# Performance work log

Hardware: AMD Instinct MI355X
Metric: run time of the kernel (lower is better)

The kernel has to match this reference:

```python
import jax, jax.numpy as jnp
import numpy as np

HID = 1024
HEADS = 16
HEAD_DIM = HID // HEADS
INTER = 4 * HID
EPS = 1e-6
SCALE = 1.0 / np.sqrt(HEAD_DIM)


def setup_inputs() -> dict:
    key = jax.random.key(0)
    ks = jax.random.split(key, 8)
    s = 0.02
    return {
        "x": jax.random.normal(ks[0], (2, 2048, HID), dtype=jnp.float32),
        "wq": jax.random.normal(ks[1], (HID, HID), dtype=jnp.float32) * s,
        "wk": jax.random.normal(ks[2], (HID, HID), dtype=jnp.float32) * s,
        "wv": jax.random.normal(ks[3], (HID, HID), dtype=jnp.float32) * s,
        "wo": jax.random.normal(ks[4], (HID, HID), dtype=jnp.float32) * s,
        "w_gate": jax.random.normal(ks[5], (INTER, HID), dtype=jnp.float32) * s,
        "w_up": jax.random.normal(ks[6], (INTER, HID), dtype=jnp.float32) * s,
        "w_down": jax.random.normal(ks[7], (HID, INTER), dtype=jnp.float32) * s,
        "norm1_w": jnp.ones((HID,), dtype=jnp.float32),
        "norm2_w": jnp.ones((HID,), dtype=jnp.float32),
    }


def _rmsnorm(x, w):
    rms = jnp.sqrt(jnp.mean(x * x, axis=-1, keepdims=True) + EPS)
    return x / rms * w


def reference(x, wq, wk, wv, wo, w_gate, w_up, w_down, norm1_w, norm2_w):
    b, s, _ = x.shape
    residual = x
    h = _rmsnorm(x, norm1_w)
    # projections: nn.Linear computes h @ W.T
    q = (h @ wq.T).reshape(b, s, HEADS, HEAD_DIM).transpose(0, 2, 1, 3)
    k = (h @ wk.T).reshape(b, s, HEADS, HEAD_DIM).transpose(0, 2, 1, 3)
    v = (h @ wv.T).reshape(b, s, HEADS, HEAD_DIM).transpose(0, 2, 1, 3)
    scores = jnp.einsum("bhqd,bhkd->bhqk", q, k) * SCALE
    attn = jax.nn.softmax(scores, axis=-1)
    out = jnp.einsum("bhqk,bhkd->bhqd", attn, v)
    out = out.transpose(0, 2, 1, 3).reshape(b, s, HID)
    x = residual + out @ wo.T
    residual = x
    h = _rmsnorm(x, norm2_w)
    gate = jax.nn.silu(h @ w_gate.T)
    up = h @ w_up.T
    mlp_out = (gate * up) @ w_down.T
    return residual + mlp_out
```

## Files before the change

kernel.cpp:

```cpp
#include <hip/hip_runtime.h>
#include <hip/hip_bf16.h>

#define HID 1024
#define SEQ 2048
#define NTOK 4096
#define ATT_SCALE 0.125f

typedef __attribute__((ext_vector_type(4))) float f32x4;
typedef __attribute__((ext_vector_type(16))) float f32x16;
typedef __attribute__((ext_vector_type(8))) __bf16 bf16x8;
typedef __attribute__((ext_vector_type(4))) __bf16 bf16x4;
typedef __bf16 bf16;

__device__ __forceinline__ bf16 f2bf(float f) { return (bf16)f; }

__device__ __forceinline__ void gld_lds16(const void* g, void* l) {
  __builtin_amdgcn_global_load_lds((const __attribute__((address_space(1))) void*)g,
                                   (__attribute__((address_space(3))) void*)l,
                                   16, 0, 0);
}

__device__ __forceinline__ f32x4 mfma16(bf16x8 a, bf16x8 b, f32x4 c) {
  return __builtin_amdgcn_mfma_f32_16x16x32_bf16(a, b, c, 0, 0, 0);
}
__device__ __forceinline__ f32x16 mfma32(bf16x8 a, bf16x8 b, f32x16 c) {
  return __builtin_amdgcn_mfma_f32_32x32x16_bf16(a, b, c, 0, 0, 0);
}

struct CvtArgs {
  const float* src[7];
  bf16* dst[7];
};

__global__ __launch_bounds__(256) void cvt_weights(CvtArgs a) {
  const int g = blockIdx.x * 256 + threadIdx.x;
  const int s = g >> 18;
  const int seg = s < 4 ? s : (s < 8 ? 4 : (s < 12 ? 5 : 6));
  const int start = seg < 4 ? (seg << 18) : (((seg - 4) << 20) + (1 << 20));
  const int loc = (g - start) << 2;
  const float4 v = *(const float4*)(a.src[seg] + loc);
  bf16x4 o = {f2bf(v.x), f2bf(v.y), f2bf(v.z), f2bf(v.w)};
  *(bf16x4*)(a.dst[seg] + loc) = o;
}

__global__ __launch_bounds__(256) void rmsnorm_k(const float* __restrict__ x,
                                                 const float* __restrict__ w,
                                                 bf16* __restrict__ h) {
  const int row = blockIdx.x;
  const int tid = threadIdx.x;
  const float4 xv = *(const float4*)(x + (size_t)row * HID + tid * 4);
  float ss = xv.x * xv.x + xv.y * xv.y + xv.z * xv.z + xv.w * xv.w;
#pragma unroll
  for (int m = 1; m < 64; m <<= 1) ss += __shfl_xor(ss, m, 64);
  __shared__ float wsum[4];
  if ((tid & 63) == 0) wsum[tid >> 6] = ss;
  __syncthreads();
  const float tot = wsum[0] + wsum[1] + wsum[2] + wsum[3];
  const float inv = rsqrtf(tot * (1.0f / HID) + 1e-6f);
  const float4 wv = *(const float4*)(w + tid * 4);
  bf16x4 o = {f2bf(xv.x * inv * wv.x), f2bf(xv.y * inv * wv.y),
              f2bf(xv.z * inv * wv.z), f2bf(xv.w * inv * wv.w)};
  *(bf16x4*)(h + (size_t)row * HID + tid * 4) = o;
}

template <int EPI>
__global__ __launch_bounds__(256) void gemm_bt(const bf16* __restrict__ A, int lda,
                                               const bf16* __restrict__ B, int ldb,
                                               void* __restrict__ C,
                                               const float* __restrict__ R,
                                               int ldc, int K) {
  alignas(16) __shared__ bf16 As[128 * 32];
  alignas(16) __shared__ bf16 Bs[128 * 32];
  const int tid = threadIdx.x;
  const int wid = tid >> 6;
  const int lane = tid & 63;
  const int bm0 = blockIdx.y * 128;
  const int bn0 = blockIdx.x * 128;
  const int wr = wid >> 1, wc = wid & 1;

  f32x4 acc[4][4] = {};

  const int sr = tid >> 2;
  const int sc = (tid & 3) << 3;
  const bf16* gA = A + (size_t)(bm0 + sr) * lda + sc;
  const bf16* gB = B + (size_t)(bn0 + sr) * ldb + sc;
  bf16* lA = As + wid * 512;
  bf16* lB = Bs + wid * 512;
  const int frow = lane & 15;
  const int kofs = (lane >> 4) << 3;

  for (int k0 = 0; k0 < K; k0 += 32) {
    __syncthreads();
    gld_lds16(gA + k0, lA);
    gld_lds16(gA + k0 + (size_t)64 * lda, lA + 2048);
    gld_lds16(gB + k0, lB);
    gld_lds16(gB + k0 + (size_t)64 * ldb, lB + 2048);
    __syncthreads();
    bf16x8 af[4], bfr[4];
#pragma unroll
    for (int m = 0; m < 4; ++m)
      af[m] = *(const bf16x8*)(As + (wr * 64 + m * 16 + frow) * 32 + kofs);
#pragma unroll
    for (int n = 0; n < 4; ++n)
      bfr[n] = *(const bf16x8*)(Bs + (wc * 64 + n * 16 + frow) * 32 + kofs);
#pragma unroll
    for (int m = 0; m < 4; ++m)
#pragma unroll
      for (int n = 0; n < 4; ++n)
        acc[m][n] = mfma16(af[m], bfr[n], acc[m][n]);
  }

  const int er = bm0 + wr * 64 + ((lane >> 4) << 2);
  const int ec = bn0 + wc * 64 + (lane & 15);
#pragma unroll
  for (int m = 0; m < 4; ++m)
#pragma unroll
    for (int n = 0; n < 4; ++n)
#pragma unroll
      for (int r = 0; r < 4; ++r) {
        const size_t idx = (size_t)(er + m * 16 + r) * ldc + (ec + n * 16);
        if (EPI == 0) ((bf16*)C)[idx] = f2bf(acc[m][n][r]);
        else          ((float*)C)[idx] = R[idx] + acc[m][n][r];
      }
}

__global__ __launch_bounds__(256) void vtrans_k(const bf16* __restrict__ qkv,
                                                bf16* __restrict__ vt) {
  const int bh = blockIdx.y;
  const int b = bh >> 4, head = bh & 15;
  const int st0 = blockIdx.x * 64;
  const int wid = threadIdx.x >> 6, lane = threadIdx.x & 63;
  const bf16* src = qkv + ((size_t)b * SEQ + st0 + lane) * 3072 + 2 * HID + head * 64 + wid * 16;
  bf16* dst = vt + (size_t)bh * (64 * SEQ) + st0 + lane;
#pragma unroll
  for (int half = 0; half < 2; ++half) {
    bf16x8 v = *(const bf16x8*)(src + half * 8);
#pragma unroll
    for (int i = 0; i < 8; ++i)
      dst[(size_t)(wid * 16 + half * 8 + i) * SEQ] = v[i];
  }
}

__global__ __launch_bounds__(128) void attn_k(const bf16* __restrict__ qkv,
                                              const bf16* __restrict__ vt,
                                              bf16* __restrict__ attn_out) {
  const int bh = blockIdx.y;
  const int b = bh >> 4, head = bh & 15;
  const int tid = threadIdx.x, wid = tid >> 6, lane = tid & 63;
  const int l31 = lane & 31, h = lane >> 5;
  const int r7 = l31 & 7;

  alignas(16) __shared__ bf16 Ks[64 * 64];
  alignas(16) __shared__ bf16 Vs[64 * 64];

  const size_t tokq = (size_t)b * SEQ + blockIdx.x * 64 + wid * 32 + l31;
  bf16x8 qf[4];
#pragma unroll
  for (int s = 0; s < 4; ++s) {
    bf16x8 t = *(const bf16x8*)(qkv + tokq * 3072 + head * 64 + s * 16 + h * 8);
#pragma unroll
    for (int i = 0; i < 8; ++i) t[i] = f2bf((float)t[i] * ATT_SCALE);
    qf[s] = t;
  }

  const int sr = tid >> 1;
  const int sc = (tid & 1) * 32;
  const int p5 = sr & 31;
  const int keyr = (sr & 32) | (p5 & 16) | (((p5 >> 2) & 1) << 3) | (((p5 >> 3) & 1) << 2) | (p5 & 3);
  const bf16* kg = qkv + ((size_t)b * SEQ + keyr) * 3072 + HID + head * 64 + sc;
  const bf16* vg = vt + (size_t)bh * (64 * SEQ) + (size_t)sr * SEQ + sc;
  int wofs[4];
#pragma unroll
  for (int j = 0; j < 4; ++j)
    wofs[j] = sr * 64 + ((((sc >> 3) + j) ^ (sr & 7)) << 3);

  f32x16 o0 = {}, o1 = {};
  float m = -1e30f, l = 0.f;

  for (int t0 = 0; t0 < SEQ; t0 += 64) {
    __syncthreads();
#pragma unroll
    for (int j = 0; j < 4; ++j) {
      bf16x8 kv = *(const bf16x8*)(kg + (size_t)t0 * 3072 + j * 8);
      *(bf16x8*)(Ks + wofs[j]) = kv;
      bf16x8 vv = *(const bf16x8*)(vg + t0 + j * 8);
      *(bf16x8*)(Vs + wofs[j]) = vv;
    }
    __syncthreads();

    f32x16 s0 = {}, s1 = {};
#pragma unroll
    for (int s = 0; s < 4; ++s) {
      bf16x8 k0 = *(const bf16x8*)(Ks + l31 * 64 + (((2 * s + h) ^ r7) << 3));
      s0 = mfma32(k0, qf[s], s0);
      bf16x8 k1 = *(const bf16x8*)(Ks + (32 + l31) * 64 + (((2 * s + h) ^ r7) << 3));
      s1 = mfma32(k1, qf[s], s1);
    }

    float pmax = s0[0];
#pragma unroll
    for (int i = 1; i < 16; ++i) pmax = fmaxf(pmax, s0[i]);
#pragma unroll
    for (int i = 0; i < 16; ++i) pmax = fmaxf(pmax, s1[i]);
    pmax = fmaxf(pmax, __shfl_xor(pmax, 32, 64));
    const float mnew = fmaxf(m, pmax);
    const float al = __expf(m - mnew);
    m = mnew;

    bf16x8 pa[4];
    float sum = 0.f;
#pragma unroll
    for (int t = 0; t < 2; ++t)
#pragma unroll
      for (int j = 0; j < 8; ++j) {
        const float p = __expf(s0[8 * t + j] - mnew);
        sum += p;
        pa[t][j] = f2bf(p);
      }
#pragma unroll
    for (int t = 0; t < 2; ++t)
#pragma unroll
      for (int j = 0; j < 8; ++j) {
        const float p = __expf(s1[8 * t + j] - mnew);
        sum += p;
        pa[2 + t][j] = f2bf(p);
      }
    sum += __shfl_xor(sum, 32, 64);
    l = l * al + sum;
#pragma unroll
    for (int i = 0; i < 16; ++i) { o0[i] *= al; o1[i] *= al; }

#pragma unroll
    for (int t = 0; t < 4; ++t) {
      bf16x8 v0 = *(const bf16x8*)(Vs + l31 * 64 + (((2 * t + h) ^ r7) << 3));
      o0 = mfma32(v0, pa[t], o0);
      bf16x8 v1 = *(const bf16x8*)(Vs + (32 + l31) * 64 + (((2 * t + h) ^ r7) << 3));
      o1 = mfma32(v1, pa[t], o1);
    }
  }

  const float inv = 1.0f / l;
  bf16* obase = attn_out + tokq * HID + head * 64;
#pragma unroll
  for (int rq = 0; rq < 4; ++rq) {
    bf16x4 w0, w1;
#pragma unroll
    for (int i = 0; i < 4; ++i) {
      w0[i] = f2bf(o0[4 * rq + i] * inv);
      w1[i] = f2bf(o1[4 * rq + i] * inv);
    }
    *(bf16x4*)(obase + 8 * rq + 4 * h) = w0;
    *(bf16x4*)(obase + 32 + 8 * rq + 4 * h) = w1;
  }
}

__global__ __launch_bounds__(256) void silu_mul_k(bf16* __restrict__ gu) {
  const int t = blockIdx.x * 256 + threadIdx.x;
  const int row = t >> 9;
  const int j = (t & 511) << 3;
  bf16* p = gu + (size_t)row * 8192 + j;
  bf16x8 g8 = *(const bf16x8*)p;
  bf16x8 u8 = *(const bf16x8*)(p + 4096);
  bf16x8 o;
#pragma unroll
  for (int i = 0; i < 8; ++i) {
    const float g = (float)g8[i], u = (float)u8[i];
    const float s = g / (1.0f + __expf(-g));
    o[i] = f2bf(s * u);
  }
  *(bf16x8*)p = o;
}

extern "C" void kernel_launch(void* const* d_in, const int* in_sizes, int n_in,
                              void* d_out, int out_size, void* d_ws, size_t ws_size,
                              hipStream_t stream) {
  const float* x  = (const float*)d_in[0];
  const float* wq = (const float*)d_in[1];
  const float* wk = (const float*)d_in[2];
  const float* wv = (const float*)d_in[3];
  const float* wo = (const float*)d_in[4];
  const float* wg = (const float*)d_in[5];
  const float* wu = (const float*)d_in[6];
  const float* wd = (const float*)d_in[7];
  const float* n1 = (const float*)d_in[8];
  const float* n2 = (const float*)d_in[9];

  char* ws = (char*)d_ws;
  bf16* wqkv_b  = (bf16*)(ws);
  bf16* wo_b    = (bf16*)(ws + 6291456);
  bf16* wgu_b   = (bf16*)(ws + 8388608);
  bf16* wd_b    = (bf16*)(ws + 25165824);
  bf16* h       = (bf16*)(ws + 33554432);
  bf16* attnout = (bf16*)(ws + 41943040);
  bf16* qkv     = (bf16*)(ws + 50331648);
  bf16* vt      = (bf16*)(ws + 75497472);
  bf16* gu      = (bf16*)(ws + 50331648);
  float* x2     = (float*)d_out;

  CvtArgs ca;
  ca.src[0] = wq; ca.dst[0] = wqkv_b;
  ca.src[1] = wk; ca.dst[1] = wqkv_b + 1048576;
  ca.src[2] = wv; ca.dst[2] = wqkv_b + 2097152;
  ca.src[3] = wo; ca.dst[3] = wo_b;
  ca.src[4] = wg; ca.dst[4] = wgu_b;
  ca.src[5] = wu; ca.dst[5] = wgu_b + 4194304;
  ca.src[6] = wd; ca.dst[6] = wd_b;

  cvt_weights<<<dim3(16384), dim3(256), 0, stream>>>(ca);
  rmsnorm_k<<<dim3(NTOK), dim3(256), 0, stream>>>(x, n1, h);
  gemm_bt<0><<<dim3(24, 32), dim3(256), 0, stream>>>(h, 1024, wqkv_b, 1024,
                                                     (void*)qkv, (const float*)nullptr, 3072, 1024);
  vtrans_k<<<dim3(32, 32), dim3(256), 0, stream>>>(qkv, vt);
  attn_k<<<dim3(32, 32), dim3(128), 0, stream>>>(qkv, vt, attnout);
  gemm_bt<1><<<dim3(8, 32), dim3(256), 0, stream>>>(attnout, 1024, wo_b, 1024,
                                                    (void*)x2, x, 1024, 1024);
  rmsnorm_k<<<dim3(NTOK), dim3(256), 0, stream>>>(x2, n2, h);
  gemm_bt<0><<<dim3(64, 32), dim3(256), 0, stream>>>(h, 1024, wgu_b, 1024,
                                                     (void*)gu, (const float*)nullptr, 8192, 1024);
  silu_mul_k<<<dim3(8192), dim3(256), 0, stream>>>(gu);
  gemm_bt<1><<<dim3(8, 32), dim3(256), 0, stream>>>(gu, 8192, wd_b, 4096,
                                                    (void*)d_out, (const float*)x2, 1024, 4096);
}
```

Baseline: 472.4 us.

## Add 256x256 double-buffered swizzled GEMM for QKV and gate/up projections

Introduces a new 512-thread GEMM kernel with 256x256 output tiles, K-step 64, double-buffered LDS filled via direct global-to-LDS loads, and XOR-swizzled LDS layout. It replaces the 128x128 gemm_bt for the QKV and gate/up projections. The larger tiles raise arithmetic intensity and the double buffering overlaps loads with MFMA work. In exchange, LDS use is high (128KB per block) and the grid has fewer blocks (192 for QKV), which may under-fill the 256 CUs for that GEMM.

```diff
diff --git a/kernel.cpp b/kernel.cpp
--- a/kernel.cpp
+++ b/kernel.cpp
@@ -61,6 +61,96 @@
   bf16x4 o = {f2bf(xv.x * inv * wv.x), f2bf(xv.y * inv * wv.y),
               f2bf(xv.z * inv * wv.z), f2bf(xv.w * inv * wv.w)};
   *(bf16x4*)(h + (size_t)row * HID + tid * 4) = o;
+}
+
+__global__ __launch_bounds__(512, 2) void gemm256(const bf16* __restrict__ A,
+                                                  const bf16* __restrict__ B,
+                                                  bf16* __restrict__ C,
+                                                  int N, int K) {
+  alignas(16) __shared__ bf16 As[2][256][64];
+  alignas(16) __shared__ bf16 Bs[2][256][64];
+  const int tid = threadIdx.x;
+  const int wid = tid >> 6, lane = tid & 63;
+  const int wm = wid >> 2, wn = wid & 3;
+  const int bm0 = blockIdx.y << 8, bn0 = blockIdx.x << 8;
+
+  const int srow = (wid << 3) + (lane >> 3);
+  const int gch = ((lane & 7) ^ (lane >> 3)) << 3;
+  const bf16* gA = A + (size_t)(bm0 + srow) * K + gch;
+  const bf16* gB = B + (size_t)(bn0 + srow) * K + gch;
+
+  const int fr = lane & 15, fc = lane >> 4, fx = lane & 7;
+
+  f32x4 acc[8][4] = {};
+  const int nt = K >> 6;
+
+  auto stage = [&](int c, int k0) {
+#pragma unroll
+    for (int i = 0; i < 4; ++i)
+      gld_lds16(gA + (size_t)(i * 64) * K + k0, &As[c][i * 64 + (wid << 3)][0]);
+#pragma unroll
+    for (int i = 0; i < 4; ++i)
+      gld_lds16(gB + (size_t)(i * 64) * K + k0, &Bs[c][i * 64 + (wid << 3)][0]);
+  };
+
+  stage(0, 0);
+  stage(1, 64);
+  asm volatile("s_waitcnt vmcnt(8)" ::: "memory");
+  __builtin_amdgcn_s_barrier();
+  __builtin_amdgcn_sched_barrier(0);
+
+  for (int t = 0; t < nt; ++t) {
+    const int c = t & 1;
+    bf16x8 bfrag[2][4];
+#pragma unroll
+    for (int s = 0; s < 2; ++s)
+#pragma unroll
+      for (int n = 0; n < 4; ++n)
+        bfrag[s][n] = *(const bf16x8*)&Bs[c][wn * 64 + n * 16 + fr]
+                                         [(((s << 2) + fc) ^ fx) << 3];
+#pragma unroll
+    for (int q = 0; q < 4; ++q) {
+      bf16x8 af[2][2];
+#pragma unroll
+      for (int mi = 0; mi < 2; ++mi)
+#pragma unroll
+        for (int s = 0; s < 2; ++s)
+          af[mi][s] = *(const bf16x8*)&As[c][wm * 128 + (q * 2 + mi) * 16 + fr]
+                                           [(((s << 2) + fc) ^ fx) << 3];
+      __builtin_amdgcn_s_setprio(1);
+#pragma unroll
+      for (int mi = 0; mi < 2; ++mi)
+#pragma unroll
+        for (int n = 0; n < 4; ++n)
+#pragma unroll
+          for (int s = 0; s < 2; ++s)
+            acc[q * 2 + mi][n] = mfma16(af[mi][s], bfrag[s][n], acc[q * 2 + mi][n]);
+      __builtin_amdgcn_s_setprio(0);
+    }
+    __builtin_amdgcn_sched_barrier(0);
+    __builtin_amdgcn_s_barrier();
+    __builtin_amdgcn_sched_barrier(0);
+    if (t + 2 < nt) {
+      stage(c, (t + 2) << 6);
+      asm volatile("s_waitcnt vmcnt(8)" ::: "memory");
+    } else {
+      asm volatile("s_waitcnt vmcnt(0)" ::: "memory");
+    }
+    __builtin_amdgcn_s_barrier();
+    __builtin_amdgcn_sched_barrier(0);
+  }
+
+#pragma unroll
+  for (int m = 0; m < 8; ++m) {
+    const int row = bm0 + wm * 128 + m * 16 + (fc << 2);
+#pragma unroll
+    for (int n = 0; n < 4; ++n) {
+      const int col = bn0 + wn * 64 + n * 16 + fr;
+#pragma unroll
+      for (int r = 0; r < 4; ++r)
+        C[(size_t)(row + r) * N + col] = f2bf(acc[m][n][r]);
+    }
+  }
 }
 
 template <int EPI>
@@ -308,15 +398,13 @@
 
   cvt_weights<<<dim3(16384), dim3(256), 0, stream>>>(ca);
   rmsnorm_k<<<dim3(NTOK), dim3(256), 0, stream>>>(x, n1, h);
-  gemm_bt<0><<<dim3(24, 32), dim3(256), 0, stream>>>(h, 1024, wqkv_b, 1024,
-                                                     (void*)qkv, (const float*)nullptr, 3072, 1024);
+  gemm256<<<dim3(12, 16), dim3(512), 0, stream>>>(h, wqkv_b, qkv, 3072, 1024);
   vtrans_k<<<dim3(32, 32), dim3(256), 0, stream>>>(qkv, vt);
   attn_k<<<dim3(32, 32), dim3(128), 0, stream>>>(qkv, vt, attnout);
   gemm_bt<1><<<dim3(8, 32), dim3(256), 0, stream>>>(attnout, 1024, wo_b, 1024,
                                                     (void*)x2, x, 1024, 1024);
   rmsnorm_k<<<dim3(NTOK), dim3(256), 0, stream>>>(x2, n2, h);
-  gemm_bt<0><<<dim3(64, 32), dim3(256), 0, stream>>>(h, 1024, wgu_b, 1024,
-                                                     (void*)gu, (const float*)nullptr, 8192, 1024);
+  gemm256<<<dim3(32, 16), dim3(512), 0, stream>>>(h, wgu_b, gu, 8192, 1024);
   silu_mul_k<<<dim3(8192), dim3(256), 0, stream>>>(gu);
   gemm_bt<1><<<dim3(8, 32), dim3(256), 0, stream>>>(gu, 8192, wd_b, 4096,
                                                     (void*)d_out, (const float*)x2, 1024, 4096);
```

Measured after the change: 460.0 us. 2.6% less time.
